# Optimization experiments

Measured on AMD Instinct MI355X. Metric: run time of the kernel, lower is better.

The kernel has to match this reference:

```python
import jax, jax.numpy as jnp
import numpy as np
from jax import lax

IN_CH = 256
OUT_CH = 256
INTER = IN_CH // 2
KERNEL = 3


def setup_inputs() -> dict:
    key = jax.random.key(0)
    ks = jax.random.split(key, 6)
    B, C, H, W = 8, IN_CH, 128, 128
    x = jax.random.normal(ks[0], (B, C, H, W), dtype=jnp.float32)
    s = 1.0 / np.sqrt(C)
    Wq = jax.random.normal(ks[1], (INTER, C), dtype=jnp.float32) * s
    Wk = jax.random.normal(ks[2], (INTER, C), dtype=jnp.float32) * s
    Wv = jax.random.normal(ks[3], (INTER, C), dtype=jnp.float32) * s
    w1d = jax.random.normal(ks[4], (KERNEL,), dtype=jnp.float32) * (1.0 / np.sqrt(KERNEL))
    Wc = jax.random.normal(ks[5], (OUT_CH, INTER, 3, 3), dtype=jnp.float32) * (1.0 / np.sqrt(INTER * 9))
    return {"x": x, "Wq": Wq, "Wk": Wk, "Wv": Wv, "w1d": w1d, "Wc": Wc}


def reference(x, Wq, Wk, Wv, w1d, Wc):
    B, C, H, W = x.shape
    inter = Wq.shape[0]
    Hs, Ws = H // 4, W // 4  # 1x1 conv, stride 4, pad 0 == spatial subsample
    xs = x[:, :, ::4, ::4]  # [B, C, Hs, Ws]
    q = jnp.einsum('oc,bchw->bohw', Wq, xs).reshape(B, inter, Hs * Ws)  # [B, inter, N]
    k = jnp.einsum('oc,bchw->bohw', Wk, xs).reshape(B, inter, Hs * Ws)
    v = jnp.einsum('oc,bchw->bohw', Wv, xs).reshape(B, inter, Hs * Ws)
    # gate = softmax(Q^T K) over last dim, shape [B, N, N]
    scores = jnp.einsum('bcn,bcm->bnm', q, k)
    gate = jax.nn.softmax(scores, axis=-1)
    # gated value: [B, inter, N] -> [B, inter, Hs, Ws]
    gv = jnp.einsum('bnm,bcm->bcn', gate, v).reshape(B, inter, Hs, Ws)
    # ECA channel gating: global avg pool -> conv1d over channel dim -> sigmoid
    ca = gv.mean(axis=(2, 3))  # [B, inter]
    ca = lax.conv_general_dilated(
        ca[:, None, :],                     # [B, 1, inter]
        w1d[None, None, :],                 # [1, 1, K]
        window_strides=(1,), padding=[((KERNEL - 1) // 2,) * 2],
        dimension_numbers=('NCH', 'OIH', 'NCH'))
    ca = jax.nn.sigmoid(ca)[:, 0, :, None, None]  # [B, inter, 1, 1]
    out = gv * ca
    out = lax.conv_general_dilated(
        out, Wc, window_strides=(1, 1), padding='SAME',
        dimension_numbers=('NCHW', 'OIHW', 'NCHW'))
    return out, gate, ca
```

## Files before the change

### kernel.cpp

```cpp
#include <hip/hip_runtime.h>
#include <math.h>

#define B_   8
#define C_   256
#define CI_  128
#define N_   1024
#define HW_  32
#define CO_  256

typedef __bf16 v8bf __attribute__((ext_vector_type(8)));
typedef float  f32x4 __attribute__((ext_vector_type(4)));
typedef unsigned short ushort_t;

__device__ __forceinline__ unsigned short f2bf_rne(float f) {
    unsigned int u = __float_as_uint(f);
    unsigned int r = u + 0x7FFF + ((u >> 16) & 1);
    return (unsigned short)(r >> 16);
}
__device__ __forceinline__ float bf2f(unsigned short h) {
    return __uint_as_float(((unsigned int)h) << 16);
}
__device__ __forceinline__ v8bf ld8(const ushort_t* p) {
    return *(const v8bf*)p;
}

__global__ __launch_bounds__(256) void prep_w_kernel(
    const float* __restrict__ Wc,
    const float* __restrict__ Wq, const float* __restrict__ Wk,
    const float* __restrict__ Wv,
    ushort_t* __restrict__ Whi, ushort_t* __restrict__ Wlo,
    ushort_t* __restrict__ Wp_hi, ushort_t* __restrict__ Wp_lo)
{
    if (blockIdx.x < 1152) {
        int idx = blockIdx.x * 256 + threadIdx.x;
        int o = idx / 1152;
        int r = idx - o * 1152;
        int ci = r / 9;
        int tap = r - ci * 9;
        float v = Wc[idx];
        unsigned short h = f2bf_rne(v);
        unsigned short l = f2bf_rne(v - bf2f(h));
        int didx = o * 1152 + tap * 128 + ci;
        Whi[didx] = h; Wlo[didx] = l;
    } else {
        int j = (blockIdx.x - 1152) * 256 + threadIdx.x;
        int o = j >> 8, c = j & 255;
        float v = (o < 128) ? Wq[o * 256 + c]
                : (o < 256) ? Wk[(o - 128) * 256 + c]
                            : Wv[(o - 256) * 256 + c];
        unsigned short h = f2bf_rne(v);
        unsigned short l = f2bf_rne(v - bf2f(h));
        Wp_hi[j] = h; Wp_lo[j] = l;
    }
}

__global__ __launch_bounds__(256) void prep_x_kernel(
    const float* __restrict__ x,
    ushort_t* __restrict__ xs_hi, ushort_t* __restrict__ xs_lo)
{
    __shared__ ushort_t lh[32 * 264];
    __shared__ ushort_t ll[32 * 264];
    const int h = blockIdx.x, b = blockIdx.y;
    const int tid = threadIdx.x;
    const int w = tid & 31, cg = tid >> 5;
    for (int c0 = 0; c0 < 256; c0 += 8) {
        int c = c0 + cg;
        float v = x[((size_t)(b * C_ + c) * 128 + h * 4) * 128 + w * 4];
        unsigned short hi = f2bf_rne(v);
        unsigned short lo = f2bf_rne(v - bf2f(hi));
        lh[w * 264 + c] = hi;
        ll[w * 264 + c] = lo;
    }
    __syncthreads();
    const int ww = tid >> 3, cs = tid & 7;
    size_t dst = ((size_t)(b * N_) + h * 32 + ww) * 256 + cs * 32;
    #pragma unroll
    for (int t = 0; t < 4; ++t) {
        *(uint4*)&xs_hi[dst + t * 8] = *(uint4*)&lh[ww * 264 + cs * 32 + t * 8];
        *(uint4*)&xs_lo[dst + t * 8] = *(uint4*)&ll[ww * 264 + cs * 32 + t * 8];
    }
}

__global__ __launch_bounds__(256) void proj_mfma_kernel(
    const ushort_t* __restrict__ Wp_hi, const ushort_t* __restrict__ Wp_lo,
    const ushort_t* __restrict__ xs_hi, const ushort_t* __restrict__ xs_lo,
    ushort_t* __restrict__ qt_hi, ushort_t* __restrict__ qt_lo,
    ushort_t* __restrict__ kt_hi, ushort_t* __restrict__ kt_lo,
    ushort_t* __restrict__ vB_hi, ushort_t* __restrict__ vB_lo)
{
    const int n0 = blockIdx.x * 64;
    const int o0 = blockIdx.y * 64;
    const int b  = blockIdx.z;
    const int tid = threadIdx.x;
    const int l = tid & 63, wv = tid >> 6;
    const int wy = wv >> 1, wx = wv & 1;
    const int ln = l & 15, quad = l >> 4;

    f32x4 acc[2][2];
    #pragma unroll
    for (int i = 0; i < 2; ++i)
        #pragma unroll
        for (int j = 0; j < 2; ++j) acc[i][j] = (f32x4){0.f,0.f,0.f,0.f};

    const ushort_t* Ah_p[2]; const ushort_t* Al_p[2];
    const ushort_t* Bh_p[2]; const ushort_t* Bl_p[2];
    #pragma unroll
    for (int i = 0; i < 2; ++i) {
        size_t off = (size_t)(o0 + wy * 32 + i * 16 + ln) * 256 + quad * 8;
        Ah_p[i] = Wp_hi + off; Al_p[i] = Wp_lo + off;
    }
    #pragma unroll
    for (int j = 0; j < 2; ++j) {
        size_t off = ((size_t)(b * N_) + n0 + wx * 32 + j * 16 + ln) * 256 + quad * 8;
        Bh_p[j] = xs_hi + off; Bl_p[j] = xs_lo + off;
    }

    #pragma unroll 4
    for (int k0 = 0; k0 < 256; k0 += 32) {
        v8bf Ah[2], Al[2], Bh[2], Bl[2];
        #pragma unroll
        for (int i = 0; i < 2; ++i) { Ah[i] = ld8(Ah_p[i] + k0); Al[i] = ld8(Al_p[i] + k0); }
        #pragma unroll
        for (int j = 0; j < 2; ++j) { Bh[j] = ld8(Bh_p[j] + k0); Bl[j] = ld8(Bl_p[j] + k0); }
        #pragma unroll
        for (int i = 0; i < 2; ++i)
            #pragma unroll
            for (int j = 0; j < 2; ++j) {
                acc[i][j] = __builtin_amdgcn_mfma_f32_16x16x32_bf16(Ah[i], Bh[j], acc[i][j], 0, 0, 0);
                acc[i][j] = __builtin_amdgcn_mfma_f32_16x16x32_bf16(Ah[i], Bl[j], acc[i][j], 0, 0, 0);
                acc[i][j] = __builtin_amdgcn_mfma_f32_16x16x32_bf16(Al[i], Bh[j], acc[i][j], 0, 0, 0);
            }
    }

    if (o0 < 256) {
        ushort_t* th = (o0 < 128) ? qt_hi : kt_hi;
        ushort_t* tl = (o0 < 128) ? qt_lo : kt_lo;
        const int ob = o0 & 127;
        #pragma unroll
        for (int i = 0; i < 2; ++i)
            #pragma unroll
            for (int j = 0; j < 2; ++j) {
                int oo = ob + wy * 32 + i * 16 + quad * 4;
                int n  = n0 + wx * 32 + j * 16 + ln;
                unsigned int h01 = 0, h23 = 0, l01 = 0, l23 = 0;
                #pragma unroll
                for (int r = 0; r < 4; ++r) {
                    float f = acc[i][j][r];
                    unsigned short hh = f2bf_rne(f);
                    unsigned short lo = f2bf_rne(f - bf2f(hh));
                    if (r < 2) { h01 |= ((unsigned)hh) << (16 * r); l01 |= ((unsigned)lo) << (16 * r); }
                    else       { h23 |= ((unsigned)hh) << (16 * (r - 2)); l23 |= ((unsigned)lo) << (16 * (r - 2)); }
                }
                size_t off = ((size_t)(b * N_) + n) * 128 + oo;
                *(uint2*)&th[off] = make_uint2(h01, h23);
                *(uint2*)&tl[off] = make_uint2(l01, l23);
            }
    } else {
        #pragma unroll
        for (int i = 0; i < 2; ++i)
            #pragma unroll
            for (int j = 0; j < 2; ++j)
                #pragma unroll
                for (int r = 0; r < 4; ++r) {
                    int c = (o0 - 256) + wy * 32 + i * 16 + quad * 4 + r;
                    int m = n0 + wx * 32 + j * 16 + ln;
                    float f = acc[i][j][r];
                    unsigned short hh = f2bf_rne(f);
                    unsigned short lo = f2bf_rne(f - bf2f(hh));
                    size_t off = (((size_t)b * 32 + (m >> 5)) * 128 + c) * 32 + (m & 31);
                    vB_hi[off] = hh; vB_lo[off] = lo;
                }
    }
}

__global__ __launch_bounds__(256, 1) void attn_fused_kernel(
    const ushort_t* __restrict__ qt_hi, const ushort_t* __restrict__ qt_lo,
    const ushort_t* __restrict__ kt_hi, const ushort_t* __restrict__ kt_lo,
    const ushort_t* __restrict__ vB_hi, const ushort_t* __restrict__ vB_lo,
    float* __restrict__ gate, float* __restrict__ gv)
{
    __shared__ __align__(16) char gsm[65536];
    __shared__ float redA[4][32];
    __shared__ float redB[4][32];

    const int n0 = blockIdx.x * 32;
    const int b  = blockIdx.y;
    const int tid = threadIdx.x;
    const int l = tid & 63, w = tid >> 6;
    const int ln = l & 15, quad = l >> 4;
    const int Mw = w * 256;

    const ushort_t* qb_h = qt_hi + ((size_t)(b * N_) + n0) * 128;
    const ushort_t* qb_l = qt_lo + ((size_t)(b * N_) + n0) * 128;
    const ushort_t* kb_h = kt_hi + (size_t)(b * N_) * 128;
    const ushort_t* kb_l = kt_lo + (size_t)(b * N_) * 128;

    f32x4 acc[2][16];
    #pragma unroll
    for (int nt = 0; nt < 2; ++nt)
        #pragma unroll
        for (int mt = 0; mt < 16; ++mt) acc[nt][mt] = (f32x4){0.f,0.f,0.f,0.f};

    #pragma unroll
    for (int c0 = 0; c0 < 128; c0 += 32) {
        v8bf Ah[2], Al[2];
        #pragma unroll
        for (int nt = 0; nt < 2; ++nt) {
            size_t aoff = (size_t)(nt * 16 + ln) * 128 + c0 + quad * 8;
            Ah[nt] = ld8(qb_h + aoff); Al[nt] = ld8(qb_l + aoff);
        }
        #pragma unroll
        for (int mt = 0; mt < 16; ++mt) {
            size_t boff = (size_t)(Mw + mt * 16 + ln) * 128 + c0 + quad * 8;
            v8bf Bh = ld8(kb_h + boff);
            v8bf Bl = ld8(kb_l + boff);
            #pragma unroll
            for (int nt = 0; nt < 2; ++nt) {
                acc[nt][mt] = __builtin_amdgcn_mfma_f32_16x16x32_bf16(Ah[nt], Bh, acc[nt][mt], 0, 0, 0);
                acc[nt][mt] = __builtin_amdgcn_mfma_f32_16x16x32_bf16(Ah[nt], Bl, acc[nt][mt], 0, 0, 0);
                acc[nt][mt] = __builtin_amdgcn_mfma_f32_16x16x32_bf16(Al[nt], Bh, acc[nt][mt], 0, 0, 0);
            }
        }
    }

    float rmax[2][4];
    #pragma unroll
    for (int nt = 0; nt < 2; ++nt)
        #pragma unroll
        for (int r = 0; r < 4; ++r) {
            float m = acc[nt][0][r];
            #pragma unroll
            for (int mt = 1; mt < 16; ++mt) m = fmaxf(m, acc[nt][mt][r]);
            rmax[nt][r] = m;
        }
    #pragma unroll
    for (int nt = 0; nt < 2; ++nt)
        #pragma unroll
        for (int r = 0; r < 4; ++r) {
            float m = rmax[nt][r];
            #pragma unroll
            for (int xm = 1; xm <= 8; xm <<= 1) m = fmaxf(m, __shfl_xor(m, xm, 64));
            rmax[nt][r] = m;
        }
    if (ln == 0) {
        #pragma unroll
        for (int nt = 0; nt < 2; ++nt)
            #pragma unroll
            for (int r = 0; r < 4; ++r)
                redA[w][nt * 16 + quad * 4 + r] = rmax[nt][r];
    }
    __syncthreads();
    #pragma unroll
    for (int nt = 0; nt < 2; ++nt)
        #pragma unroll
        for (int r = 0; r < 4; ++r) {
            int row = nt * 16 + quad * 4 + r;
            rmax[nt][r] = fmaxf(fmaxf(redA[0][row], redA[1][row]),
                                fmaxf(redA[2][row], redA[3][row]));
        }

    float rsum[2][4];
    #pragma unroll
    for (int nt = 0; nt < 2; ++nt)
        #pragma unroll
        for (int r = 0; r < 4; ++r) {
            float s = 0.f;
            #pragma unroll
            for (int mt = 0; mt < 16; ++mt) {
                float e = __expf(acc[nt][mt][r] - rmax[nt][r]);
                acc[nt][mt][r] = e;
                s += e;
            }
            rsum[nt][r] = s;
        }
    #pragma unroll
    for (int nt = 0; nt < 2; ++nt)
        #pragma unroll
        for (int r = 0; r < 4; ++r) {
            float s = rsum[nt][r];
            #pragma unroll
            for (int xm = 1; xm <= 8; xm <<= 1) s += __shfl_xor(s, xm, 64);
            rsum[nt][r] = s;
        }
    if (ln == 0) {
        #pragma unroll
        for (int nt = 0; nt < 2; ++nt)
            #pragma unroll
            for (int r = 0; r < 4; ++r)
                redB[w][nt * 16 + quad * 4 + r] = rsum[nt][r];
    }
    __syncthreads();
    #pragma unroll
    for (int nt = 0; nt < 2; ++nt)
        #pragma unroll
        for (int r = 0; r < 4; ++r) {
            int row = nt * 16 + quad * 4 + r;
            float inv = 1.0f / (redB[0][row] + redB[1][row] + redB[2][row] + redB[3][row]);
            #pragma unroll
            for (int mt = 0; mt < 16; ++mt) acc[nt][mt][r] *= inv;
        }

    float* grow = gate + (size_t)b * N_ * N_;
    #pragma unroll
    for (int nt = 0; nt < 2; ++nt)
        #pragma unroll
        for (int r = 0; r < 4; ++r) {
            int n  = n0 + nt * 16 + quad * 4 + r;
            int nl = nt * 16 + quad * 4 + r;
            #pragma unroll
            for (int mt = 0; mt < 16; ++mt) {
                int m = Mw + mt * 16 + ln;
                float v = acc[nt][mt][r];
                grow[(size_t)n * N_ + m] = v;
                int chunk = m >> 3;
                int addr = nl * 2048 + (((chunk ^ (nl & 7))) << 4) + ((m & 7) << 1);
                *(ushort_t*)&gsm[addr] = f2bf_rne(v);
            }
        }
    __syncthreads();

    const ushort_t* vb_h = vB_hi + (size_t)b * CI_ * N_;
    const ushort_t* vb_l = vB_lo + (size_t)b * CI_ * N_;

    f32x4 acc2[2][2];
    #pragma unroll
    for (int ct = 0; ct < 2; ++ct)
        #pragma unroll
        for (int nt = 0; nt < 2; ++nt) acc2[ct][nt] = (f32x4){0.f,0.f,0.f,0.f};

    #pragma unroll 4
    for (int m0 = 0; m0 < 1024; m0 += 32) {
        v8bf Bg[2];
        #pragma unroll
        for (int nt = 0; nt < 2; ++nt) {
            int nl = nt * 16 + ln;
            int chunk = (m0 >> 3) + quad;
            Bg[nt] = *(const v8bf*)&gsm[nl * 2048 + (((chunk ^ (nl & 7))) << 4)];
        }
        #pragma unroll
        for (int ct = 0; ct < 2; ++ct) {
            int c = w * 32 + ct * 16 + ln;
            size_t aoff = (((size_t)(m0 >> 5)) * 128 + c) * 32 + quad * 8;
            v8bf Avh = ld8(vb_h + aoff);
            v8bf Avl = ld8(vb_l + aoff);
            #pragma unroll
            for (int nt = 0; nt < 2; ++nt) {
                acc2[ct][nt] = __builtin_amdgcn_mfma_f32_16x16x32_bf16(Avh, Bg[nt], acc2[ct][nt], 0, 0, 0);
                acc2[ct][nt] = __builtin_amdgcn_mfma_f32_16x16x32_bf16(Avl, Bg[nt], acc2[ct][nt], 0, 0, 0);
            }
        }
    }

    #pragma unroll
    for (int ct = 0; ct < 2; ++ct)
        #pragma unroll
        for (int nt = 0; nt < 2; ++nt)
            #pragma unroll
            for (int r = 0; r < 4; ++r) {
                int c = w * 32 + ct * 16 + quad * 4 + r;
                int n = n0 + nt * 16 + ln;
                gv[(size_t)(b * CI_ + c) * N_ + n] = acc2[ct][nt][r];
            }
}

__global__ __launch_bounds__(256) void mean_kernel(
    const float* __restrict__ gv, float* __restrict__ meanb)
{
    const int i = blockIdx.x, b = blockIdx.y;
    const int tid = threadIdx.x;
    const int wid = tid >> 6, lane = tid & 63;
    __shared__ float red[4];
    const float* base = gv + (size_t)(b * CI_ + i) * N_;
    float4 v = ((const float4*)base)[tid];
    float s = v.x + v.y + v.z + v.w;
    #pragma unroll
    for (int off = 32; off; off >>= 1) s += __shfl_xor(s, off, 64);
    if (lane == 0) red[wid] = s;
    __syncthreads();
    if (tid == 0)
        meanb[b * CI_ + i] = (red[0] + red[1] + red[2] + red[3]) * (1.0f / 1024.0f);
}

__global__ __launch_bounds__(1024) void ca_kernel(
    const float* __restrict__ meanb, const float* __restrict__ w1d,
    float* __restrict__ ca)
{
    const int t = threadIdx.x;
    const int i = t & 127;
    float left  = (i > 0)   ? meanb[t - 1] : 0.0f;
    float mid   = meanb[t];
    float right = (i < 127) ? meanb[t + 1] : 0.0f;
    float val = w1d[0] * left + w1d[1] * mid + w1d[2] * right;
    ca[t] = 1.0f / (1.0f + __expf(-val));
}

#define BHI 0
#define BLO 17408
#define AHI 34816
#define ALO 43008
__global__ __launch_bounds__(256) void conv_mfma_kernel(
    const float* __restrict__ gv, const float* __restrict__ ca,
    const ushort_t* __restrict__ Whi, const ushort_t* __restrict__ Wlo,
    float* __restrict__ out)
{
    __shared__ char smem[51200];
    const int b   = blockIdx.z;
    const int h0  = blockIdx.y * 2;
    const int o0  = blockIdx.x * 64;
    const int tid = threadIdx.x;
    const int l   = tid & 63;
    const int wv  = tid >> 6;
    const int wy  = wv >> 1;
    const int wx  = wv & 1;
    const int ln  = l & 15;
    const int quad = l >> 4;

    f32x4 acc[2][2];
    #pragma unroll
    for (int i = 0; i < 2; ++i)
        #pragma unroll
        for (int j = 0; j < 2; ++j)
            acc[i][j] = (f32x4){0.f, 0.f, 0.f, 0.f};

    for (int half = 0; half < 2; ++half) {
        __syncthreads();
        for (int u = tid; u < 136 * 16; u += 256) {
            int p   = u >> 4;
            int ciq = u & 15;
            int hrel = p / 34;
            int c    = p - hrel * 34;
            int gr = h0 + hrel - 1;
            int gc = c - 1;
            bool ok = ((unsigned)gr < 32u) && ((unsigned)gc < 32u);
            int cib = half * 64 + ciq * 4;
            unsigned int hx = 0, hy = 0, lx = 0, ly = 0;
            #pragma unroll
            for (int t = 0; t < 4; ++t) {
                float v = 0.0f;
                if (ok)
                    v = gv[(size_t)(b * CI_ + cib + t) * N_ + gr * 32 + gc]
                        * ca[b * CI_ + cib + t];
                unsigned short h = f2bf_rne(v);
                unsigned short lo = f2bf_rne(v - bf2f(h));
                if (t < 2) { hx |= ((unsigned)h) << (16 * t); lx |= ((unsigned)lo) << (16 * t); }
                else       { hy |= ((unsigned)h) << (16 * (t - 2)); ly |= ((unsigned)lo) << (16 * (t - 2)); }
            }
            int addr = p * 128 + (((ciq >> 1) ^ (p & 7)) << 4) + ((ciq & 1) << 3);
            *(uint2*)&smem[BHI + addr] = make_uint2(hx, hy);
            *(uint2*)&smem[BLO + addr] = make_uint2(lx, ly);
        }
        for (int tap = 0; tap < 9; ++tap) {
            __syncthreads();
            #pragma unroll
            for (int it = 0; it < 2; ++it) {
                int row = it * 32 + (tid >> 3);
                int s   = tid & 7;
                int csrc = s ^ (row & 7);
                size_t gsrc = (size_t)(o0 + row) * 1152 + tap * 128 + half * 64 + csrc * 8;
                int la = row * 128 + s * 16;
                *(uint4*)&smem[AHI + la] = *(const uint4*)&Whi[gsrc];
                *(uint4*)&smem[ALO + la] = *(const uint4*)&Wlo[gsrc];
            }
            __syncthreads();
            const int dy = tap / 3, dx = tap - dy * 3;
            const int pbase = (wx + dy) * 34 + dx;
            #pragma unroll
            for (int cc = 0; cc < 2; ++cc) {
                v8bf Bh[2], Bl[2], Ah[2], Al[2];
                #pragma unroll
                for (int j = 0; j < 2; ++j) {
                    int p = pbase + j * 16 + ln;
                    int ch = cc * 4 + quad;
                    int addr = p * 128 + ((ch ^ (p & 7)) << 4);
                    Bh[j] = *(const v8bf*)&smem[BHI + addr];
                    Bl[j] = *(const v8bf*)&smem[BLO + addr];
                }
                #pragma unroll
                for (int i = 0; i < 2; ++i) {
                    int o = wy * 32 + i * 16 + ln;
                    int ch = cc * 4 + quad;
                    int addr = o * 128 + ((ch ^ (o & 7)) << 4);
                    Ah[i] = *(const v8bf*)&smem[AHI + addr];
                    Al[i] = *(const v8bf*)&smem[ALO + addr];
                }
                #pragma unroll
                for (int i = 0; i < 2; ++i)
                    #pragma unroll
                    for (int j = 0; j < 2; ++j) {
                        acc[i][j] = __builtin_amdgcn_mfma_f32_16x16x32_bf16(Ah[i], Bh[j], acc[i][j], 0, 0, 0);
                        acc[i][j] = __builtin_amdgcn_mfma_f32_16x16x32_bf16(Ah[i], Bl[j], acc[i][j], 0, 0, 0);
                        acc[i][j] = __builtin_amdgcn_mfma_f32_16x16x32_bf16(Al[i], Bh[j], acc[i][j], 0, 0, 0);
                    }
            }
        }
    }

    const int h = h0 + wx;
    #pragma unroll
    for (int i = 0; i < 2; ++i)
        #pragma unroll
        for (int j = 0; j < 2; ++j)
            #pragma unroll
            for (int r = 0; r < 4; ++r) {
                int o = o0 + wy * 32 + i * 16 + quad * 4 + r;
                int w = j * 16 + ln;
                out[(size_t)(b * CO_ + o) * N_ + h * 32 + w] = acc[i][j][r];
            }
}

extern "C" void kernel_launch(void* const* d_in, const int* in_sizes, int n_in,
                              void* d_out, int out_size, void* d_ws, size_t ws_size,
                              hipStream_t stream) {
    const float* x   = (const float*)d_in[0];
    const float* Wq  = (const float*)d_in[1];
    const float* Wk  = (const float*)d_in[2];
    const float* Wv  = (const float*)d_in[3];
    const float* w1d = (const float*)d_in[4];
    const float* Wc  = (const float*)d_in[5];

    float* out  = (float*)d_out;
    float* gate = out + 2097152;
    float* ca   = gate + 8388608;

    float*    gv      = (float*)d_ws;
    float*    meanb   = gv + 1048576;
    ushort_t* Whi     = (ushort_t*)(meanb + 1024);
    ushort_t* Wlo     = Whi + 294912;
    ushort_t* Wp_hi   = Wlo + 294912;
    ushort_t* Wp_lo   = Wp_hi + 98304;
    ushort_t* xs_hi   = Wp_lo + 98304;
    ushort_t* xs_lo   = xs_hi + 2097152;
    ushort_t* qt_hi   = xs_lo + 2097152;
    ushort_t* qt_lo   = qt_hi + 1048576;
    ushort_t* kt_hi   = qt_lo + 1048576;
    ushort_t* kt_lo   = kt_hi + 1048576;
    ushort_t* vB_hi   = kt_lo + 1048576;
    ushort_t* vB_lo   = vB_hi + 1048576;

    prep_w_kernel<<<dim3(1536), 256, 0, stream>>>(Wc, Wq, Wk, Wv, Whi, Wlo, Wp_hi, Wp_lo);
    prep_x_kernel<<<dim3(32, 8), 256, 0, stream>>>(x, xs_hi, xs_lo);
    proj_mfma_kernel<<<dim3(16, 6, 8), 256, 0, stream>>>(
        Wp_hi, Wp_lo, xs_hi, xs_lo, qt_hi, qt_lo, kt_hi, kt_lo, vB_hi, vB_lo);
    attn_fused_kernel<<<dim3(32, 8), 256, 0, stream>>>(
        qt_hi, qt_lo, kt_hi, kt_lo, vB_hi, vB_lo, gate, gv);
    mean_kernel<<<dim3(128, 8), 256, 0, stream>>>(gv, meanb);
    ca_kernel<<<1, 1024, 0, stream>>>(meanb, w1d, ca);
    conv_mfma_kernel<<<dim3(4, 16, 8), 256, 0, stream>>>(gv, ca, Whi, Wlo, out);
}
```

Measured before the change: 304.4 us.

## Halve attention row tile, fuse mean into attention, load conv weights directly

The attention kernel now handles 16 query rows per block instead of 32, which doubles the grid to 512 blocks and allows two blocks per CU. Its epilogue computes the channel mean with shuffles and atomicAdd into a zeroed buffer, so the separate mean kernel is gone. The conv kernel stops staging weights through shared memory for each tap and reads them straight from global memory into registers, which removes two barriers per tap. In exchange, K and V are re-read more per query row, the atomics make the float summation order nondeterministic, and weight loads are no longer coalesced through LDS.

Result: slower. 336.5 us (+10.6%).

```diff
diff --git a/kernel.cpp b/kernel.cpp
--- a/kernel.cpp
+++ b/kernel.cpp
@@ -173,17 +173,17 @@
     }
 }
 
-__global__ __launch_bounds__(256, 1) void attn_fused_kernel(
+__global__ __launch_bounds__(256, 2) void attn_fused_kernel(
     const ushort_t* __restrict__ qt_hi, const ushort_t* __restrict__ qt_lo,
     const ushort_t* __restrict__ kt_hi, const ushort_t* __restrict__ kt_lo,
     const ushort_t* __restrict__ vB_hi, const ushort_t* __restrict__ vB_lo,
-    float* __restrict__ gate, float* __restrict__ gv)
-{
-    __shared__ __align__(16) char gsm[65536];
-    __shared__ float redA[4][32];
-    __shared__ float redB[4][32];
-
-    const int n0 = blockIdx.x * 32;
+    float* __restrict__ gate, float* __restrict__ gv, float* __restrict__ meanb)
+{
+    __shared__ __align__(16) char gsm[32768];
+    __shared__ float redA[4][16];
+    __shared__ float redB[4][16];
+
+    const int n0 = blockIdx.x * 16;
     const int b  = blockIdx.y;
     const int tid = threadIdx.x;
     const int l = tid & 63, w = tid >> 6;
@@ -195,190 +195,129 @@
     const ushort_t* kb_h = kt_hi + (size_t)(b * N_) * 128;
     const ushort_t* kb_l = kt_lo + (size_t)(b * N_) * 128;
 
-    f32x4 acc[2][16];
-    #pragma unroll
-    for (int nt = 0; nt < 2; ++nt)
-        #pragma unroll
-        for (int mt = 0; mt < 16; ++mt) acc[nt][mt] = (f32x4){0.f,0.f,0.f,0.f};
+    f32x4 acc[16];
+    #pragma unroll
+    for (int mt = 0; mt < 16; ++mt) acc[mt] = (f32x4){0.f,0.f,0.f,0.f};
 
     #pragma unroll
     for (int c0 = 0; c0 < 128; c0 += 32) {
-        v8bf Ah[2], Al[2];
-        #pragma unroll
-        for (int nt = 0; nt < 2; ++nt) {
-            size_t aoff = (size_t)(nt * 16 + ln) * 128 + c0 + quad * 8;
-            Ah[nt] = ld8(qb_h + aoff); Al[nt] = ld8(qb_l + aoff);
-        }
+        size_t aoff = (size_t)ln * 128 + c0 + quad * 8;
+        v8bf Ah = ld8(qb_h + aoff);
+        v8bf Al = ld8(qb_l + aoff);
         #pragma unroll
         for (int mt = 0; mt < 16; ++mt) {
             size_t boff = (size_t)(Mw + mt * 16 + ln) * 128 + c0 + quad * 8;
             v8bf Bh = ld8(kb_h + boff);
             v8bf Bl = ld8(kb_l + boff);
-            #pragma unroll
-            for (int nt = 0; nt < 2; ++nt) {
-                acc[nt][mt] = __builtin_amdgcn_mfma_f32_16x16x32_bf16(Ah[nt], Bh, acc[nt][mt], 0, 0, 0);
-                acc[nt][mt] = __builtin_amdgcn_mfma_f32_16x16x32_bf16(Ah[nt], Bl, acc[nt][mt], 0, 0, 0);
-                acc[nt][mt] = __builtin_amdgcn_mfma_f32_16x16x32_bf16(Al[nt], Bh, acc[nt][mt], 0, 0, 0);
-            }
-        }
-    }
-
-    float rmax[2][4];
-    #pragma unroll
-    for (int nt = 0; nt < 2; ++nt)
-        #pragma unroll
-        for (int r = 0; r < 4; ++r) {
-            float m = acc[nt][0][r];
-            #pragma unroll
-            for (int mt = 1; mt < 16; ++mt) m = fmaxf(m, acc[nt][mt][r]);
-            rmax[nt][r] = m;
-        }
-    #pragma unroll
-    for (int nt = 0; nt < 2; ++nt)
-        #pragma unroll
-        for (int r = 0; r < 4; ++r) {
-            float m = rmax[nt][r];
-            #pragma unroll
-            for (int xm = 1; xm <= 8; xm <<= 1) m = fmaxf(m, __shfl_xor(m, xm, 64));
-            rmax[nt][r] = m;
-        }
+            acc[mt] = __builtin_amdgcn_mfma_f32_16x16x32_bf16(Ah, Bh, acc[mt], 0, 0, 0);
+            acc[mt] = __builtin_amdgcn_mfma_f32_16x16x32_bf16(Ah, Bl, acc[mt], 0, 0, 0);
+            acc[mt] = __builtin_amdgcn_mfma_f32_16x16x32_bf16(Al, Bh, acc[mt], 0, 0, 0);
+        }
+    }
+
+    float rmax[4];
+    #pragma unroll
+    for (int r = 0; r < 4; ++r) {
+        float m = acc[0][r];
+        #pragma unroll
+        for (int mt = 1; mt < 16; ++mt) m = fmaxf(m, acc[mt][r]);
+        #pragma unroll
+        for (int xm = 1; xm <= 8; xm <<= 1) m = fmaxf(m, __shfl_xor(m, xm, 64));
+        rmax[r] = m;
+    }
     if (ln == 0) {
         #pragma unroll
-        for (int nt = 0; nt < 2; ++nt)
-            #pragma unroll
-            for (int r = 0; r < 4; ++r)
-                redA[w][nt * 16 + quad * 4 + r] = rmax[nt][r];
+        for (int r = 0; r < 4; ++r) redA[w][quad * 4 + r] = rmax[r];
     }
     __syncthreads();
     #pragma unroll
-    for (int nt = 0; nt < 2; ++nt)
-        #pragma unroll
-        for (int r = 0; r < 4; ++r) {
-            int row = nt * 16 + quad * 4 + r;
-            rmax[nt][r] = fmaxf(fmaxf(redA[0][row], redA[1][row]),
-                                fmaxf(redA[2][row], redA[3][row]));
-        }
-
-    float rsum[2][4];
-    #pragma unroll
-    for (int nt = 0; nt < 2; ++nt)
-        #pragma unroll
-        for (int r = 0; r < 4; ++r) {
-            float s = 0.f;
-            #pragma unroll
-            for (int mt = 0; mt < 16; ++mt) {
-                float e = __expf(acc[nt][mt][r] - rmax[nt][r]);
-                acc[nt][mt][r] = e;
-                s += e;
-            }
-            rsum[nt][r] = s;
-        }
-    #pragma unroll
-    for (int nt = 0; nt < 2; ++nt)
-        #pragma unroll
-        for (int r = 0; r < 4; ++r) {
-            float s = rsum[nt][r];
-            #pragma unroll
-            for (int xm = 1; xm <= 8; xm <<= 1) s += __shfl_xor(s, xm, 64);
-            rsum[nt][r] = s;
-        }
+    for (int r = 0; r < 4; ++r) {
+        int row = quad * 4 + r;
+        rmax[r] = fmaxf(fmaxf(redA[0][row], redA[1][row]),
+                        fmaxf(redA[2][row], redA[3][row]));
+    }
+
+    float rsum[4];
+    #pragma unroll
+    for (int r = 0; r < 4; ++r) {
+        float s = 0.f;
+        #pragma unroll
+        for (int mt = 0; mt < 16; ++mt) {
+            float e = __expf(acc[mt][r] - rmax[r]);
+            acc[mt][r] = e;
+            s += e;
+        }
+        #pragma unroll
+        for (int xm = 1; xm <= 8; xm <<= 1) s += __shfl_xor(s, xm, 64);
+        rsum[r] = s;
+    }
     if (ln == 0) {
         #pragma unroll
-        for (int nt = 0; nt < 2; ++nt)
-            #pragma unroll
-            for (int r = 0; r < 4; ++r)
-                redB[w][nt * 16 + quad * 4 + r] = rsum[nt][r];
+        for (int r = 0; r < 4; ++r) redB[w][quad * 4 + r] = rsum[r];
     }
     __syncthreads();
     #pragma unroll
-    for (int nt = 0; nt < 2; ++nt)
-        #pragma unroll
-        for (int r = 0; r < 4; ++r) {
-            int row = nt * 16 + quad * 4 + r;
-            float inv = 1.0f / (redB[0][row] + redB[1][row] + redB[2][row] + redB[3][row]);
-            #pragma unroll
-            for (int mt = 0; mt < 16; ++mt) acc[nt][mt][r] *= inv;
-        }
+    for (int r = 0; r < 4; ++r) {
+        int row = quad * 4 + r;
+        float inv = 1.0f / (redB[0][row] + redB[1][row] + redB[2][row] + redB[3][row]);
+        #pragma unroll
+        for (int mt = 0; mt < 16; ++mt) acc[mt][r] *= inv;
+    }
 
     float* grow = gate + (size_t)b * N_ * N_;
     #pragma unroll
-    for (int nt = 0; nt < 2; ++nt)
-        #pragma unroll
-        for (int r = 0; r < 4; ++r) {
-            int n  = n0 + nt * 16 + quad * 4 + r;
-            int nl = nt * 16 + quad * 4 + r;
-            #pragma unroll
-            for (int mt = 0; mt < 16; ++mt) {
-                int m = Mw + mt * 16 + ln;
-                float v = acc[nt][mt][r];
-                grow[(size_t)n * N_ + m] = v;
-                int chunk = m >> 3;
-                int addr = nl * 2048 + (((chunk ^ (nl & 7))) << 4) + ((m & 7) << 1);
-                *(ushort_t*)&gsm[addr] = f2bf_rne(v);
-            }
-        }
+    for (int r = 0; r < 4; ++r) {
+        int nl = quad * 4 + r;
+        int n  = n0 + nl;
+        #pragma unroll
+        for (int mt = 0; mt < 16; ++mt) {
+            int m = Mw + mt * 16 + ln;
+            float v = acc[mt][r];
+            grow[(size_t)n * N_ + m] = v;
+            int chunk = m >> 3;
+            int addr = nl * 2048 + (((chunk ^ (nl & 7))) << 4) + ((m & 7) << 1);
+            *(ushort_t*)&gsm[addr] = f2bf_rne(v);
+        }
+    }
     __syncthreads();
 
     const ushort_t* vb_h = vB_hi + (size_t)b * CI_ * N_;
     const ushort_t* vb_l = vB_lo + (size_t)b * CI_ * N_;
 
-    f32x4 acc2[2][2];
-    #pragma unroll
-    for (int ct = 0; ct < 2; ++ct)
-        #pragma unroll
-        for (int nt = 0; nt < 2; ++nt) acc2[ct][nt] = (f32x4){0.f,0.f,0.f,0.f};
+    f32x4 acc2[2];
+    acc2[0] = (f32x4){0.f,0.f,0.f,0.f};
+    acc2[1] = (f32x4){0.f,0.f,0.f,0.f};
 
     #pragma unroll 4
     for (int m0 = 0; m0 < 1024; m0 += 32) {
-        v8bf Bg[2];
-        #pragma unroll
-        for (int nt = 0; nt < 2; ++nt) {
-            int nl = nt * 16 + ln;
-            int chunk = (m0 >> 3) + quad;
-            Bg[nt] = *(const v8bf*)&gsm[nl * 2048 + (((chunk ^ (nl & 7))) << 4)];
-        }
+        int nl = ln;
+        int chunk = (m0 >> 3) + quad;
+        v8bf Bg = *(const v8bf*)&gsm[nl * 2048 + (((chunk ^ (nl & 7))) << 4)];
         #pragma unroll
         for (int ct = 0; ct < 2; ++ct) {
             int c = w * 32 + ct * 16 + ln;
             size_t aoff = (((size_t)(m0 >> 5)) * 128 + c) * 32 + quad * 8;
             v8bf Avh = ld8(vb_h + aoff);
             v8bf Avl = ld8(vb_l + aoff);
-            #pragma unroll
-            for (int nt = 0; nt < 2; ++nt) {
-                acc2[ct][nt] = __builtin_amdgcn_mfma_f32_16x16x32_bf16(Avh, Bg[nt], acc2[ct][nt], 0, 0, 0);
-                acc2[ct][nt] = __builtin_amdgcn_mfma_f32_16x16x32_bf16(Avl, Bg[nt], acc2[ct][nt], 0, 0, 0);
-            }
+            acc2[ct] = __builtin_amdgcn_mfma_f32_16x16x32_bf16(Avh, Bg, acc2[ct], 0, 0, 0);
+            acc2[ct] = __builtin_amdgcn_mfma_f32_16x16x32_bf16(Avl, Bg, acc2[ct], 0, 0, 0);
         }
     }
 
     #pragma unroll
     for (int ct = 0; ct < 2; ++ct)
         #pragma unroll
-        for (int nt = 0; nt < 2; ++nt)
-            #pragma unroll
-            for (int r = 0; r < 4; ++r) {
-                int c = w * 32 + ct * 16 + quad * 4 + r;
-                int n = n0 + nt * 16 + ln;
-                gv[(size_t)(b * CI_ + c) * N_ + n] = acc2[ct][nt][r];
-            }
-}
-
-__global__ __launch_bounds__(256) void mean_kernel(
-    const float* __restrict__ gv, float* __restrict__ meanb)
-{
-    const int i = blockIdx.x, b = blockIdx.y;
-    const int tid = threadIdx.x;
-    const int wid = tid >> 6, lane = tid & 63;
-    __shared__ float red[4];
-    const float* base = gv + (size_t)(b * CI_ + i) * N_;
-    float4 v = ((const float4*)base)[tid];
-    float s = v.x + v.y + v.z + v.w;
-    #pragma unroll
-    for (int off = 32; off; off >>= 1) s += __shfl_xor(s, off, 64);
-    if (lane == 0) red[wid] = s;
-    __syncthreads();
-    if (tid == 0)
-        meanb[b * CI_ + i] = (red[0] + red[1] + red[2] + red[3]) * (1.0f / 1024.0f);
+        for (int r = 0; r < 4; ++r) {
+            int c = w * 32 + ct * 16 + quad * 4 + r;
+            int n = n0 + ln;
+            float v = acc2[ct][r];
+            gv[(size_t)(b * CI_ + c) * N_ + n] = v;
+            float s = v;
+            #pragma unroll
+            for (int xm = 1; xm <= 8; xm <<= 1) s += __shfl_xor(s, xm, 64);
+            if (ln == 0)
+                atomicAdd(&meanb[b * CI_ + c], s * (1.0f / 1024.0f));
+        }
 }
 
 __global__ __launch_bounds__(1024) void ca_kernel(
@@ -396,14 +335,12 @@
 
 #define BHI 0
 #define BLO 17408
-#define AHI 34816
-#define ALO 43008
 __global__ __launch_bounds__(256) void conv_mfma_kernel(
     const float* __restrict__ gv, const float* __restrict__ ca,
     const ushort_t* __restrict__ Whi, const ushort_t* __restrict__ Wlo,
     float* __restrict__ out)
 {
-    __shared__ char smem[51200];
+    __shared__ char smem[34816];
     const int b   = blockIdx.z;
     const int h0  = blockIdx.y * 2;
     const int o0  = blockIdx.x * 64;
@@ -449,24 +386,21 @@
             *(uint2*)&smem[BHI + addr] = make_uint2(hx, hy);
             *(uint2*)&smem[BLO + addr] = make_uint2(lx, ly);
         }
+        __syncthreads();
+
         for (int tap = 0; tap < 9; ++tap) {
-            __syncthreads();
-            #pragma unroll
-            for (int it = 0; it < 2; ++it) {
-                int row = it * 32 + (tid >> 3);
-                int s   = tid & 7;
-                int csrc = s ^ (row & 7);
-                size_t gsrc = (size_t)(o0 + row) * 1152 + tap * 128 + half * 64 + csrc * 8;
-                int la = row * 128 + s * 16;
-                *(uint4*)&smem[AHI + la] = *(const uint4*)&Whi[gsrc];
-                *(uint4*)&smem[ALO + la] = *(const uint4*)&Wlo[gsrc];
-            }
-            __syncthreads();
             const int dy = tap / 3, dx = tap - dy * 3;
             const int pbase = (wx + dy) * 34 + dx;
             #pragma unroll
             for (int cc = 0; cc < 2; ++cc) {
                 v8bf Bh[2], Bl[2], Ah[2], Al[2];
+                #pragma unroll
+                for (int i = 0; i < 2; ++i) {
+                    size_t aoff = (size_t)(o0 + wy * 32 + i * 16 + ln) * 1152
+                                + tap * 128 + half * 64 + cc * 32 + quad * 8;
+                    Ah[i] = ld8(Whi + aoff);
+                    Al[i] = ld8(Wlo + aoff);
+                }
                 #pragma unroll
                 for (int j = 0; j < 2; ++j) {
                     int p = pbase + j * 16 + ln;
@@ -474,14 +408,6 @@
                     int addr = p * 128 + ((ch ^ (p & 7)) << 4);
                     Bh[j] = *(const v8bf*)&smem[BHI + addr];
                     Bl[j] = *(const v8bf*)&smem[BLO + addr];
-                }
-                #pragma unroll
-                for (int i = 0; i < 2; ++i) {
-                    int o = wy * 32 + i * 16 + ln;
-                    int ch = cc * 4 + quad;
-                    int addr = o * 128 + ((ch ^ (o & 7)) << 4);
-                    Ah[i] = *(const v8bf*)&smem[AHI + addr];
-                    Al[i] = *(const v8bf*)&smem[ALO + addr];
                 }
                 #pragma unroll
                 for (int i = 0; i < 2; ++i)
@@ -539,11 +465,11 @@
 
     prep_w_kernel<<<dim3(1536), 256, 0, stream>>>(Wc, Wq, Wk, Wv, Whi, Wlo, Wp_hi, Wp_lo);
     prep_x_kernel<<<dim3(32, 8), 256, 0, stream>>>(x, xs_hi, xs_lo);
+    hipMemsetAsync(meanb, 0, 1024 * sizeof(float), stream);
     proj_mfma_kernel<<<dim3(16, 6, 8), 256, 0, stream>>>(
         Wp_hi, Wp_lo, xs_hi, xs_lo, qt_hi, qt_lo, kt_hi, kt_lo, vB_hi, vB_lo);
-    attn_fused_kernel<<<dim3(32, 8), 256, 0, stream>>>(
-        qt_hi, qt_lo, kt_hi, kt_lo, vB_hi, vB_lo, gate, gv);
-    mean_kernel<<<dim3(128, 8), 256, 0, stream>>>(gv, meanb);
+    attn_fused_kernel<<<dim3(64, 8), 256, 0, stream>>>(
+        qt_hi, qt_lo, kt_hi, kt_lo, vB_hi, vB_lo, gate, gv, meanb);
     ca_kernel<<<1, 1024, 0, stream>>>(meanb, w1d, ca);
     conv_mfma_kernel<<<dim3(4, 16, 8), 256, 0, stream>>>(gv, ca, Whi, Wlo, out);
 }
```
